# Performance work log

Measured on AMD Instinct MI355X. Metric: run time of the kernel, lower is better.

Reference implementation:

```python
import jax, jax.numpy as jnp
import numpy as np

B, T, C = 4, 128, 512
NH, HS = 8, 64          # n_head, head_dim = C // NH
ORDER = 3               # attention_order
SCALE = 1.0 / np.sqrt(HS)


def setup_inputs() -> dict:
    key = jax.random.key(0)
    ks = jax.random.split(key, 7)
    s = 0.02
    return {
        "x": jax.random.normal(ks[0], (B, T, C), jnp.float32),
        "Wp0": jax.random.normal(ks[1], (C, C), jnp.float32) * s,
        "Wp1": jax.random.normal(ks[2], (C, C), jnp.float32) * s,
        "Wp2": jax.random.normal(ks[3], (C, C), jnp.float32) * s,
        "Wv0": jax.random.normal(ks[4], (HS, HS), jnp.float32) * s,
        "Wv1": jax.random.normal(ks[5], (HS, HS), jnp.float32) * s,
        "Wc": jax.random.normal(ks[6], (C, C), jnp.float32) * s,
    }


def _heads(x, W):
    # Linear then split heads: (B,T,C) -> (B,NH,T,HS)
    return (x @ W).reshape(B, T, NH, HS).transpose(0, 2, 1, 3)


def _causal_mask(t, order):
    # indices grid [T]^order, True where i0 >= i1 >= ... >= i_{order-1}
    idx = jnp.arange(t)
    g = jnp.stack(jnp.meshgrid(*([idx] * order), indexing='ij'), axis=-1)
    return jnp.all(jnp.diff(g, axis=-1) <= 0, axis=-1)


def reference(x, Wp0, Wp1, Wp2, Wv0, Wv1, Wc):
    p0 = _heads(x, Wp0)  # (B,NH,T,HS)
    p1 = _heads(x, Wp1)
    p2 = _heads(x, Wp2)

    # pairwise scores, then higher-order broadcast exactly as the torch einsum
    # ('bh...i,bhkd->bh...ik' sums the key over d and broadcasts — faithful).
    att = jnp.einsum('bhid,bhjd->bhij', p0, p1) * SCALE        # (B,NH,T,T)
    att = jnp.einsum('bh...i,bhkd->bh...ik', att, p2)          # (B,NH,T,T,T)

    mask = _causal_mask(T, ORDER)[None, None]                  # (1,1,T,T,T)
    att = jnp.where(mask, att, -jnp.inf)
    att = jax.nn.softmax(att.reshape(B, NH, T, T * T), axis=-1)

    # value tensors with broadcasted elementwise product over the order dims
    V0 = (p1 @ Wv0)[:, :, :, None, :]   # (B,NH,T,1,HS)
    V1 = (p2 @ Wv1)[:, :, None, :, :]   # (B,NH,1,T,HS)
    V = (V0 * V1).reshape(B, NH, T * T, HS)

    y = jnp.einsum('bhij,bhjd->bhid', att, V)                  # (B,NH,T,HS)
    y = y.transpose(0, 2, 1, 3).reshape(B, T, C)
    return y @ Wc
```

## Files before the change

kernel.cpp:

```cpp
#include <hip/hip_runtime.h>
#include <hip/hip_bf16.h>
#include <math.h>

#define B 4
#define T 128
#define C 512
#define NH 8
#define HS 64
#define BH (B*NH)

typedef __attribute__((ext_vector_type(8))) short bf16x8;
typedef __attribute__((ext_vector_type(4))) float f32x4;

__device__ __forceinline__ unsigned short bfc(float x) {
    return __builtin_bit_cast(unsigned short, __float2bfloat16(x));
}
__device__ __forceinline__ float b2f(unsigned short u) {
    unsigned int x = ((unsigned int)u) << 16;
    return __builtin_bit_cast(float, x);
}
__device__ __forceinline__ unsigned int pk_bf16(float a, float b) {
    return (unsigned int)bfc(a) | ((unsigned int)bfc(b) << 16);
}
__device__ __forceinline__ float lo_f(unsigned int g) {
    return __builtin_bit_cast(float, g << 16);
}
__device__ __forceinline__ float hi_f(unsigned int g) {
    return __builtin_bit_cast(float, g & 0xffff0000u);
}

__global__ __launch_bounds__(256) void prep_kernel(
    const float* __restrict__ X, const float* __restrict__ Wp0, const float* __restrict__ Wp1,
    const float* __restrict__ Wp2, const float* __restrict__ Wc,
    const float* __restrict__ Wv0, const float* __restrict__ Wv1,
    unsigned short* __restrict__ Xb, unsigned short* __restrict__ W0T, unsigned short* __restrict__ W1T,
    unsigned short* __restrict__ W2T, unsigned short* __restrict__ WcT,
    unsigned short* __restrict__ We0T, unsigned short* __restrict__ We1T)
{
    __shared__ float Ls[64][69];
    __shared__ float As[16][68];
    __shared__ float Bs[16][68];
    const int z = blockIdx.z;
    const int tid = threadIdx.x;
    if (z == 0) {
        const int r0 = blockIdx.y * 64, c0 = blockIdx.x * 64;
        #pragma unroll
        for (int it = 0; it < 2; ++it) {
            const int q = tid + it * 256;
            const int row = q >> 3, c8 = (q & 7) * 8;
            const float4 a = *(const float4*)&X[(size_t)(r0 + row) * 512 + c0 + c8];
            const float4 b = *(const float4*)&X[(size_t)(r0 + row) * 512 + c0 + c8 + 4];
            uint4 o;
            o.x = pk_bf16(a.x, a.y);
            o.y = pk_bf16(a.z, a.w);
            o.z = pk_bf16(b.x, b.y);
            o.w = pk_bf16(b.z, b.w);
            *(uint4*)&Xb[(size_t)(r0 + row) * 512 + c0 + c8] = o;
        }
        return;
    }
    if (z <= 4) {
        const int r0 = blockIdx.y * 64, c0 = blockIdx.x * 64;
        const float* W = (z == 1) ? Wp0 : (z == 2) ? Wp1 : (z == 3) ? Wp2 : Wc;
        unsigned short* WT = (z == 1) ? W0T : (z == 2) ? W1T : (z == 3) ? W2T : WcT;
        #pragma unroll
        for (int it = 0; it < 4; ++it) {
            const int q = tid + it * 256;
            const int row = q >> 4, c4 = (q & 15) * 4;
            const float4 v = *(const float4*)&W[(size_t)(r0 + row) * 512 + c0 + c4];
            Ls[row][c4 + 0] = v.x; Ls[row][c4 + 1] = v.y; Ls[row][c4 + 2] = v.z; Ls[row][c4 + 3] = v.w;
        }
        __syncthreads();
        #pragma unroll
        for (int it = 0; it < 2; ++it) {
            const int q = tid + it * 256;
            const int nrow = q >> 3, k8 = (q & 7) * 8;
            uint4 o;
            o.x = pk_bf16(Ls[k8 + 0][nrow], Ls[k8 + 1][nrow]);
            o.y = pk_bf16(Ls[k8 + 2][nrow], Ls[k8 + 3][nrow]);
            o.z = pk_bf16(Ls[k8 + 4][nrow], Ls[k8 + 5][nrow]);
            o.w = pk_bf16(Ls[k8 + 6][nrow], Ls[k8 + 7][nrow]);
            *(uint4*)&WT[(size_t)(c0 + nrow) * 512 + r0 + k8] = o;
        }
        return;
    }
    const float* A  = (z == 5) ? Wp1 : Wp2;
    const float* Wv = (z == 5) ? Wv0 : Wv1;
    unsigned short* O = (z == 5) ? We0T : We1T;
    const int h = blockIdx.x;
    const int m0 = blockIdx.y * 64;
    const int tx = tid & 15, ty = tid >> 4;
    const int arow = tid >> 2, acol = (tid & 3) * 4;
    const int brow = tid >> 4, bcol = (tid & 15) * 4;
    float acc[4][4] = {};
    for (int k0 = 0; k0 < 64; k0 += 16) {
        const float4 av = *(const float4*)&A[(size_t)(m0 + arow) * 512 + h * 64 + k0 + acol];
        const float4 bv = *(const float4*)&Wv[(size_t)(k0 + brow) * 64 + bcol];
        __syncthreads();
        As[acol + 0][arow] = av.x; As[acol + 1][arow] = av.y;
        As[acol + 2][arow] = av.z; As[acol + 3][arow] = av.w;
        *(float4*)&Bs[brow][bcol] = bv;
        __syncthreads();
        #pragma unroll
        for (int kk = 0; kk < 16; ++kk) {
            const float4 a4 = *(const float4*)&As[kk][ty * 4];
            const float4 b4 = *(const float4*)&Bs[kk][tx * 4];
            const float ar[4] = {a4.x, a4.y, a4.z, a4.w};
            const float br[4] = {b4.x, b4.y, b4.z, b4.w};
            #pragma unroll
            for (int r = 0; r < 4; ++r)
                #pragma unroll
                for (int c = 0; c < 4; ++c)
                    acc[r][c] = fmaf(ar[r], br[c], acc[r][c]);
        }
    }
    #pragma unroll
    for (int r = 0; r < 4; ++r)
        #pragma unroll
        for (int c = 0; c < 4; ++c)
            O[(size_t)(h * 64 + tx * 4 + c) * 512 + (m0 + ty * 4 + r)] = bfc(acc[r][c]);
}

__global__ __launch_bounds__(256) void projmm_kernel(
    const unsigned short* __restrict__ Xb,
    const unsigned short* __restrict__ W0T, const unsigned short* __restrict__ W1T,
    const unsigned short* __restrict__ W2T,
    const unsigned short* __restrict__ We0T, const unsigned short* __restrict__ We1T,
    unsigned short* __restrict__ p0b, unsigned short* __restrict__ p1b,
    unsigned short* __restrict__ V0T, unsigned short* __restrict__ V1T, float* __restrict__ rr)
{
    __shared__ __align__(16) unsigned short As[64][72];
    __shared__ __align__(16) unsigned short Bs[64][72];
    __shared__ float sRS[4][64];
    const int z = blockIdx.z;
    const unsigned short* WT = (z == 0) ? W0T : (z == 1) ? W1T : (z == 2) ? W2T : (z == 3) ? We0T : We1T;
    const int m0 = blockIdx.y * 64, n0 = blockIdx.x * 64;
    const int tid = threadIdx.x;
    const int w = tid >> 6, lane = tid & 63, quad = lane >> 4, l16 = lane & 15;
    f32x4 acc[4];
    #pragma unroll
    for (int mt = 0; mt < 4; ++mt) acc[mt] = (f32x4){0.f, 0.f, 0.f, 0.f};
    for (int k0 = 0; k0 < 512; k0 += 64) {
        __syncthreads();
        #pragma unroll
        for (int it = 0; it < 2; ++it) {
            const int q = tid + it * 256;
            const int row = q >> 3, c8 = (q & 7) * 8;
            *(uint4*)&As[row][c8] = *(const uint4*)&Xb[(size_t)(m0 + row) * 512 + k0 + c8];
            *(uint4*)&Bs[row][c8] = *(const uint4*)&WT[(size_t)(n0 + row) * 512 + k0 + c8];
        }
        __syncthreads();
        #pragma unroll
        for (int kt = 0; kt < 2; ++kt) {
            const bf16x8 b8 = *(const bf16x8*)&Bs[w * 16 + l16][kt * 32 + quad * 8];
            #pragma unroll
            for (int mt = 0; mt < 4; ++mt) {
                const bf16x8 a8 = *(const bf16x8*)&As[mt * 16 + l16][kt * 32 + quad * 8];
                acc[mt] = __builtin_amdgcn_mfma_f32_16x16x32_bf16(a8, b8, acc[mt], 0, 0, 0);
            }
        }
    }
    if (z == 2) {
        #pragma unroll
        for (int mt = 0; mt < 4; ++mt)
            #pragma unroll
            for (int r = 0; r < 4; ++r) {
                float v = acc[mt][r];
                v += __shfl_xor(v, 1, 64); v += __shfl_xor(v, 2, 64);
                v += __shfl_xor(v, 4, 64); v += __shfl_xor(v, 8, 64);
                if (l16 == 0) sRS[w][mt * 16 + quad * 4 + r] = v;
            }
        __syncthreads();
        if (tid < 64) {
            const float s = sRS[0][tid] + sRS[1][tid] + sRS[2][tid] + sRS[3][tid];
            const int m = m0 + tid, b = m >> 7, tl = m & 127, h = n0 >> 6;
            rr[(b * NH + h) * T + tl] = s;
        }
        return;
    }
    const int n = n0 + w * 16 + l16;
    const int h = n >> 6, d = n & 63;
    #pragma unroll
    for (int mt = 0; mt < 4; ++mt) {
        #pragma unroll
        for (int r = 0; r < 4; ++r) {
            const int m = m0 + mt * 16 + quad * 4 + r;
            const int b = m >> 7, t = m & 127;
            const size_t hm = (size_t)(b * NH + h) * T + t;
            const float v = acc[mt][r];
            if (z == 0)      p0b[hm * HS + d] = bfc(v);
            else if (z == 1) p1b[hm * HS + d] = bfc(v);
            else if (z == 3) V0T[((size_t)(b * NH + h) * HS + d) * T + t] = bfc(v);
            else             V1T[((size_t)(b * NH + h) * HS + d) * T + t] = bfc(v);
        }
    }
}

__global__ __launch_bounds__(256) void attn_kernel(
    const unsigned short* __restrict__ p0b, const unsigned short* __restrict__ p1b,
    const float* __restrict__ rr, const unsigned short* __restrict__ V0Tg,
    const unsigned short* __restrict__ V1Tg, unsigned short* __restrict__ Yb)
{
    __shared__ __align__(16) unsigned short sE[128 * 64];
    __shared__ float sS[128];
    __shared__ float srr[128];
    __shared__ float sZ[4];

    const int blk = blockIdx.x;
    const int bh = blk & (BH - 1);
    const int i = (T - 1) - (blk >> 5);
    const int tid = threadIdx.x;
    const int w = tid >> 6;
    const int lane = tid & 63;
    const int quad = lane >> 4;
    const int l16 = lane & 15;

    if (tid < 128) srr[tid] = rr[bh * T + tid];

    uint4 v1r[4];
    {
        const unsigned short* src = V1Tg + ((size_t)bh * HS + (w << 4) + l16) * T + (quad << 3);
        #pragma unroll
        for (int kt = 0; kt < 4; ++kt) v1r[kt] = *(const uint4*)(src + (kt << 5));
    }

    {
        const unsigned short* ap = p0b + ((size_t)bh * T + i) * HS + (quad << 3);
        const unsigned short* bp = p1b + (size_t)bh * T * HS + (quad << 3);
        f32x4 s0 = (f32x4){0.f, 0.f, 0.f, 0.f};
        f32x4 s1 = (f32x4){0.f, 0.f, 0.f, 0.f};
        #pragma unroll
        for (int kt = 0; kt < 2; ++kt) {
            const bf16x8 a8 = *(const bf16x8*)(ap + (kt << 5));
            const bf16x8 b0 = *(const bf16x8*)(bp + (size_t)((w << 5) + l16) * HS + (kt << 5));
            const bf16x8 b1 = *(const bf16x8*)(bp + (size_t)((w << 5) + 16 + l16) * HS + (kt << 5));
            s0 = __builtin_amdgcn_mfma_f32_16x16x32_bf16(a8, b0, s0, 0, 0, 0);
            s1 = __builtin_amdgcn_mfma_f32_16x16x32_bf16(a8, b1, s1, 0, 0, 0);
        }
        if (quad == 0) {
            sS[(w << 5) + l16]      = s0[0] * 0.125f;
            sS[(w << 5) + 16 + l16] = s1[0] * 0.125f;
        }
    }
    __syncthreads();

    float mhat;
    {
        float s0 = (lane <= i) ? fabsf(sS[lane]) : 0.f;
        float s1 = (64 + lane <= i) ? fabsf(sS[64 + lane]) : 0.f;
        float r0 = (lane <= i) ? fabsf(srr[lane]) : 0.f;
        float r1 = (64 + lane <= i) ? fabsf(srr[64 + lane]) : 0.f;
        float aS = fmaxf(s0, s1), aR = fmaxf(r0, r1);
        #pragma unroll
        for (int off = 32; off; off >>= 1) {
            aS = fmaxf(aS, __shfl_xor(aS, off, 64));
            aR = fmaxf(aR, __shfl_xor(aR, off, 64));
        }
        mhat = aS * aR;
    }

    const float L2E = 1.4426950408889634f;
    const float bexp = -mhat * L2E;
    const int mtmax = i >> 4;
    const int cc = tid & 7;
    const int rowin = tid >> 3;
    const int k0l = cc << 3;
    float zacc = 0.f;

    float rk[8];
    *(float4*)&rk[0] = *(const float4*)&srr[k0l];
    *(float4*)&rk[4] = *(const float4*)&srr[k0l + 4];
    const int npass0 = (mtmax >> 1) + 1;
    for (int p = 0; p < npass0; ++p) {
        const int jj = (p << 5) + rowin;
        uint4 o = {0u, 0u, 0u, 0u};
        if (jj <= i && k0l <= jj) {
            const float aL = sS[jj] * L2E;
            const int dlim = jj - k0l;
            float e[8];
            #pragma unroll
            for (int q = 0; q < 8; ++q) {
                const float ex = __builtin_amdgcn_exp2f(fmaf(aL, rk[q], bexp));
                e[q] = (q <= dlim) ? ex : 0.f;
                zacc += e[q];
            }
            o.x = pk_bf16(e[0], e[1]);
            o.y = pk_bf16(e[2], e[3]);
            o.z = pk_bf16(e[4], e[5]);
            o.w = pk_bf16(e[6], e[7]);
        }
        *(uint4*)&sE[(jj << 6) + ((cc ^ (jj & 7)) << 3)] = o;
    }

    f32x4 acc[8];
    #pragma unroll
    for (int mt = 0; mt < 8; ++mt) acc[mt] = (f32x4){0.f, 0.f, 0.f, 0.f};

    if (mtmax < 4) {
        #pragma unroll
        for (int off = 32; off; off >>= 1) zacc += __shfl_xor(zacc, off, 64);
        if (lane == 0) sZ[w] = zacc;
        __syncthreads();
        #pragma unroll
        for (int mt = 0; mt < 4; ++mt) {
            if (mt <= mtmax) {
                #pragma unroll
                for (int kt = 0; kt <= 1; ++kt) {
                    if (kt <= (mt >> 1)) {
                        const int swz = ((kt << 2) + quad) ^ (l16 & 7);
                        const bf16x8 a8 = *(const bf16x8*)&sE[(((mt << 4) + l16) << 6) + (swz << 3)];
                        acc[mt] = __builtin_amdgcn_mfma_f32_16x16x32_bf16(
                            a8, __builtin_bit_cast(bf16x8, v1r[kt]), acc[mt], 0, 0, 0);
                    }
                }
            }
        }
    } else {
        __syncthreads();
        #pragma unroll
        for (int mt = 0; mt < 8; ++mt) {
            if (mt <= mtmax) {
                #pragma unroll
                for (int kt = 0; kt <= 1; ++kt) {
                    if (kt <= (mt >> 1)) {
                        const int swz = ((kt << 2) + quad) ^ (l16 & 7);
                        const bf16x8 a8 = *(const bf16x8*)&sE[(((mt << 4) + l16) << 6) + (swz << 3)];
                        acc[mt] = __builtin_amdgcn_mfma_f32_16x16x32_bf16(
                            a8, __builtin_bit_cast(bf16x8, v1r[kt]), acc[mt], 0, 0, 0);
                    }
                }
            }
        }
        __syncthreads();
        *(float4*)&rk[0] = *(const float4*)&srr[64 + k0l];
        *(float4*)&rk[4] = *(const float4*)&srr[64 + k0l + 4];
        const int npass1 = ((mtmax - 4) >> 1) + 1;
        for (int p = 0; p < npass1; ++p) {
            const int jj = 64 + (p << 5) + rowin;
            uint4 o = {0u, 0u, 0u, 0u};
            if (jj <= i && 64 + k0l <= jj) {
                const float aL = sS[jj] * L2E;
                const int dlim = jj - 64 - k0l;
                float e[8];
                #pragma unroll
                for (int q = 0; q < 8; ++q) {
                    const float ex = __builtin_amdgcn_exp2f(fmaf(aL, rk[q], bexp));
                    e[q] = (q <= dlim) ? ex : 0.f;
                    zacc += e[q];
                }
                o.x = pk_bf16(e[0], e[1]);
                o.y = pk_bf16(e[2], e[3]);
                o.z = pk_bf16(e[4], e[5]);
                o.w = pk_bf16(e[6], e[7]);
            }
            *(uint4*)&sE[(jj << 6) + ((cc ^ (jj & 7)) << 3)] = o;
        }
        #pragma unroll
        for (int off = 32; off; off >>= 1) zacc += __shfl_xor(zacc, off, 64);
        if (lane == 0) sZ[w] = zacc;
        __syncthreads();
        #pragma unroll
        for (int mt = 4; mt < 8; ++mt) {
            if (mt <= mtmax) {
                #pragma unroll
                for (int kt = 2; kt <= 3; ++kt) {
                    if (kt <= (mt >> 1)) {
                        const int swz = (((kt & 1) << 2) + quad) ^ (l16 & 7);
                        const bf16x8 a8 = *(const bf16x8*)&sE[(((mt << 4) + l16) << 6) + (swz << 3)];
                        acc[mt] = __builtin_amdgcn_mfma_f32_16x16x32_bf16(
                            a8, __builtin_bit_cast(bf16x8, v1r[kt]), acc[mt], 0, 0, 0);
                    }
                }
            }
        }
    }
    const float Z = sZ[0] + sZ[1] + sZ[2] + sZ[3];

    const unsigned short* v0t = V0Tg + ((size_t)bh * HS + (w << 4) + l16) * T;
    float part = 0.f;
    #pragma unroll
    for (int mt = 0; mt < 8; ++mt) {
        if (mt < mtmax) {
            const uint2 u = *(const uint2*)&v0t[(mt << 4) + (quad << 2)];
            part = fmaf(lo_f(u.x), acc[mt][0], part);
            part = fmaf(hi_f(u.x), acc[mt][1], part);
            part = fmaf(lo_f(u.y), acc[mt][2], part);
            part = fmaf(hi_f(u.y), acc[mt][3], part);
        } else if (mt == mtmax) {
            const uint2 u = *(const uint2*)&v0t[(mt << 4) + (quad << 2)];
            const int jb = (mt << 4) + (quad << 2);
            if (jb + 0 <= i) part = fmaf(lo_f(u.x), acc[mt][0], part);
            if (jb + 1 <= i) part = fmaf(hi_f(u.x), acc[mt][1], part);
            if (jb + 2 <= i) part = fmaf(lo_f(u.y), acc[mt][2], part);
            if (jb + 3 <= i) part = fmaf(hi_f(u.y), acc[mt][3], part);
        }
    }
    part += __shfl_xor(part, 16, 64);
    part += __shfl_xor(part, 32, 64);
    if (lane < 16) {
        const int bb = bh >> 3, hh = bh & 7;
        Yb[((size_t)(bb * T + i) * C) + hh * HS + (w << 4) + l16] = bfc(part / Z);
    }
}

__global__ __launch_bounds__(256) void outmm_kernel(
    const unsigned short* __restrict__ Ab, const unsigned short* __restrict__ WT,
    float* __restrict__ OUT)
{
    __shared__ __align__(16) unsigned short As[64][72];
    __shared__ __align__(16) unsigned short Bs[64][72];
    const int m0 = blockIdx.y * 64, n0 = blockIdx.x * 64;
    const int tid = threadIdx.x;
    const int w = tid >> 6, lane = tid & 63, quad = lane >> 4, l16 = lane & 15;
    f32x4 acc[4];
    #pragma unroll
    for (int mt = 0; mt < 4; ++mt) acc[mt] = (f32x4){0.f, 0.f, 0.f, 0.f};
    for (int k0 = 0; k0 < 512; k0 += 64) {
        __syncthreads();
        #pragma unroll
        for (int it = 0; it < 2; ++it) {
            const int q = tid + it * 256;
            const int row = q >> 3, c8 = (q & 7) * 8;
            *(uint4*)&As[row][c8] = *(const uint4*)&Ab[(size_t)(m0 + row) * 512 + k0 + c8];
            *(uint4*)&Bs[row][c8] = *(const uint4*)&WT[(size_t)(n0 + row) * 512 + k0 + c8];
        }
        __syncthreads();
        #pragma unroll
        for (int kt = 0; kt < 2; ++kt) {
            const bf16x8 b8 = *(const bf16x8*)&Bs[w * 16 + l16][kt * 32 + quad * 8];
            #pragma unroll
            for (int mt = 0; mt < 4; ++mt) {
                const bf16x8 a8 = *(const bf16x8*)&As[mt * 16 + l16][kt * 32 + quad * 8];
                acc[mt] = __builtin_amdgcn_mfma_f32_16x16x32_bf16(a8, b8, acc[mt], 0, 0, 0);
            }
        }
    }
    const int n = n0 + w * 16 + l16;
    #pragma unroll
    for (int mt = 0; mt < 4; ++mt)
        #pragma unroll
        for (int r = 0; r < 4; ++r) {
            const int mrow = m0 + mt * 16 + quad * 4 + r;
            OUT[(size_t)mrow * 512 + n] = acc[mt][r];
        }
}

extern "C" void kernel_launch(void* const* d_in, const int* in_sizes, int n_in,
                              void* d_out, int out_size, void* d_ws, size_t ws_size,
                              hipStream_t stream)
{
    const float* x   = (const float*)d_in[0];
    const float* Wp0 = (const float*)d_in[1];
    const float* Wp1 = (const float*)d_in[2];
    const float* Wp2 = (const float*)d_in[3];
    const float* Wv0 = (const float*)d_in[4];
    const float* Wv1 = (const float*)d_in[5];
    const float* Wc  = (const float*)d_in[6];
    float* out = (float*)d_out;

    char* w8 = (char*)d_ws;
    const size_t HB = 512 * 1024;
    unsigned short* Xb   = (unsigned short*)(w8 + 0 * HB);
    unsigned short* W0T  = (unsigned short*)(w8 + 1 * HB);
    unsigned short* W1T  = (unsigned short*)(w8 + 2 * HB);
    unsigned short* W2T  = (unsigned short*)(w8 + 3 * HB);
    unsigned short* WcT  = (unsigned short*)(w8 + 4 * HB);
    unsigned short* We0T = (unsigned short*)(w8 + 5 * HB);
    unsigned short* We1T = (unsigned short*)(w8 + 6 * HB);
    unsigned short* p0b  = (unsigned short*)(w8 + 7 * HB);
    unsigned short* p1b  = (unsigned short*)(w8 + 8 * HB);
    unsigned short* V0T  = (unsigned short*)(w8 + 9 * HB);
    unsigned short* V1T  = (unsigned short*)(w8 + 10 * HB);
    unsigned short* Yb   = (unsigned short*)(w8 + 11 * HB);
    float*          rr   = (float*)        (w8 + 12 * HB);

    prep_kernel  <<<dim3(8, 8, 7), 256, 0, stream>>>(x, Wp0, Wp1, Wp2, Wc, Wv0, Wv1,
                                                     Xb, W0T, W1T, W2T, WcT, We0T, We1T);
    projmm_kernel<<<dim3(8, 8, 5), 256, 0, stream>>>(Xb, W0T, W1T, W2T, We0T, We1T,
                                                     p0b, p1b, V0T, V1T, rr);
    attn_kernel  <<<dim3(BH * T), 256, 0, stream>>>(p0b, p1b, rr, V0T, V1T, Yb);
    outmm_kernel <<<dim3(8, 8), 256, 0, stream>>>(Yb, WcT, out);
}
```

Baseline: 123.2 us.

## Process eight query rows per attention block with balanced row pairing

The attention kernel now handles eight query rows per block instead of one, shrinking the grid from 4096 to 512 blocks. The score MFMA computes all eight rows' scores at once, filling otherwise wasted MFMA rows, and the V1 register load is amortized across rows. Rows are picked in mirrored pairs (ig and 15-ig within alternating 16-row groups) so per-block causal work is balanced. The trade-off is less parallelism, with only 512 blocks on a many-CU GPU, and each block runs a serial loop over its rows with extra block-wide barriers.

```diff
diff --git a/kernel.cpp b/kernel.cpp
--- a/kernel.cpp
+++ b/kernel.cpp
@@ -202,13 +202,13 @@
     const unsigned short* __restrict__ V1Tg, unsigned short* __restrict__ Yb)
 {
     __shared__ __align__(16) unsigned short sE[128 * 64];
-    __shared__ float sS[128];
+    __shared__ float sS[8][128];
     __shared__ float srr[128];
     __shared__ float sZ[4];
 
-    const int blk = blockIdx.x;
-    const int bh = blk & (BH - 1);
-    const int i = (T - 1) - (blk >> 5);
+    const int bid = blockIdx.x;
+    const int bh = bid & (BH - 1);
+    const int ig = bid >> 5;
     const int tid = threadIdx.x;
     const int w = tid >> 6;
     const int lane = tid & 63;
@@ -225,7 +225,9 @@
     }
 
     {
-        const unsigned short* ap = p0b + ((size_t)bh * T + i) * HS + (quad << 3);
+        const int qr = l16 & 7;
+        const int irow = (qr & 1) ? (16 * qr + 15 - ig) : (16 * qr + ig);
+        const unsigned short* ap = p0b + ((size_t)bh * T + irow) * HS + (quad << 3);
         const unsigned short* bp = p1b + (size_t)bh * T * HS + (quad << 3);
         f32x4 s0 = (f32x4){0.f, 0.f, 0.f, 0.f};
         f32x4 s1 = (f32x4){0.f, 0.f, 0.f, 0.f};
@@ -237,110 +239,55 @@
             s0 = __builtin_amdgcn_mfma_f32_16x16x32_bf16(a8, b0, s0, 0, 0, 0);
             s1 = __builtin_amdgcn_mfma_f32_16x16x32_bf16(a8, b1, s1, 0, 0, 0);
         }
-        if (quad == 0) {
-            sS[(w << 5) + l16]      = s0[0] * 0.125f;
-            sS[(w << 5) + 16 + l16] = s1[0] * 0.125f;
+        if (quad < 2) {
+            #pragma unroll
+            for (int r = 0; r < 4; ++r) {
+                sS[quad * 4 + r][(w << 5) + l16]      = s0[r] * 0.125f;
+                sS[quad * 4 + r][(w << 5) + 16 + l16] = s1[r] * 0.125f;
+            }
         }
     }
     __syncthreads();
 
-    float mhat;
-    {
-        float s0 = (lane <= i) ? fabsf(sS[lane]) : 0.f;
-        float s1 = (64 + lane <= i) ? fabsf(sS[64 + lane]) : 0.f;
-        float r0 = (lane <= i) ? fabsf(srr[lane]) : 0.f;
-        float r1 = (64 + lane <= i) ? fabsf(srr[64 + lane]) : 0.f;
-        float aS = fmaxf(s0, s1), aR = fmaxf(r0, r1);
-        #pragma unroll
-        for (int off = 32; off; off >>= 1) {
-            aS = fmaxf(aS, __shfl_xor(aS, off, 64));
-            aR = fmaxf(aR, __shfl_xor(aR, off, 64));
-        }
-        mhat = aS * aR;
-    }
-
+    const unsigned short* v0t = V0Tg + ((size_t)bh * HS + (w << 4) + l16) * T;
     const float L2E = 1.4426950408889634f;
-    const float bexp = -mhat * L2E;
-    const int mtmax = i >> 4;
-    const int cc = tid & 7;
-    const int rowin = tid >> 3;
-    const int k0l = cc << 3;
-    float zacc = 0.f;
-
-    float rk[8];
-    *(float4*)&rk[0] = *(const float4*)&srr[k0l];
-    *(float4*)&rk[4] = *(const float4*)&srr[k0l + 4];
-    const int npass0 = (mtmax >> 1) + 1;
-    for (int p = 0; p < npass0; ++p) {
-        const int jj = (p << 5) + rowin;
-        uint4 o = {0u, 0u, 0u, 0u};
-        if (jj <= i && k0l <= jj) {
-            const float aL = sS[jj] * L2E;
-            const int dlim = jj - k0l;
-            float e[8];
-            #pragma unroll
-            for (int q = 0; q < 8; ++q) {
-                const float ex = __builtin_amdgcn_exp2f(fmaf(aL, rk[q], bexp));
-                e[q] = (q <= dlim) ? ex : 0.f;
-                zacc += e[q];
-            }
-            o.x = pk_bf16(e[0], e[1]);
-            o.y = pk_bf16(e[2], e[3]);
-            o.z = pk_bf16(e[4], e[5]);
-            o.w = pk_bf16(e[6], e[7]);
-        }
-        *(uint4*)&sE[(jj << 6) + ((cc ^ (jj & 7)) << 3)] = o;
-    }
-
-    f32x4 acc[8];
-    #pragma unroll
-    for (int mt = 0; mt < 8; ++mt) acc[mt] = (f32x4){0.f, 0.f, 0.f, 0.f};
-
-    if (mtmax < 4) {
-        #pragma unroll
-        for (int off = 32; off; off >>= 1) zacc += __shfl_xor(zacc, off, 64);
-        if (lane == 0) sZ[w] = zacc;
-        __syncthreads();
-        #pragma unroll
-        for (int mt = 0; mt < 4; ++mt) {
-            if (mt <= mtmax) {
-                #pragma unroll
-                for (int kt = 0; kt <= 1; ++kt) {
-                    if (kt <= (mt >> 1)) {
-                        const int swz = ((kt << 2) + quad) ^ (l16 & 7);
-                        const bf16x8 a8 = *(const bf16x8*)&sE[(((mt << 4) + l16) << 6) + (swz << 3)];
-                        acc[mt] = __builtin_amdgcn_mfma_f32_16x16x32_bf16(
-                            a8, __builtin_bit_cast(bf16x8, v1r[kt]), acc[mt], 0, 0, 0);
-                    }
-                }
-            }
-        }
-    } else {
-        __syncthreads();
-        #pragma unroll
-        for (int mt = 0; mt < 8; ++mt) {
-            if (mt <= mtmax) {
-                #pragma unroll
-                for (int kt = 0; kt <= 1; ++kt) {
-                    if (kt <= (mt >> 1)) {
-                        const int swz = ((kt << 2) + quad) ^ (l16 & 7);
-                        const bf16x8 a8 = *(const bf16x8*)&sE[(((mt << 4) + l16) << 6) + (swz << 3)];
-                        acc[mt] = __builtin_amdgcn_mfma_f32_16x16x32_bf16(
-                            a8, __builtin_bit_cast(bf16x8, v1r[kt]), acc[mt], 0, 0, 0);
-                    }
-                }
-            }
-        }
-        __syncthreads();
-        *(float4*)&rk[0] = *(const float4*)&srr[64 + k0l];
-        *(float4*)&rk[4] = *(const float4*)&srr[64 + k0l + 4];
-        const int npass1 = ((mtmax - 4) >> 1) + 1;
-        for (int p = 0; p < npass1; ++p) {
-            const int jj = 64 + (p << 5) + rowin;
+
+    for (int qq = 7; qq >= 0; --qq) {
+        const int i = (qq & 1) ? (16 * qq + 15 - ig) : (16 * qq + ig);
+        const float* sSq = sS[qq];
+
+        float mhat;
+        {
+            float a0 = (lane <= i) ? fabsf(sSq[lane]) : 0.f;
+            float a1 = (64 + lane <= i) ? fabsf(sSq[64 + lane]) : 0.f;
+            float r0 = (lane <= i) ? fabsf(srr[lane]) : 0.f;
+            float r1 = (64 + lane <= i) ? fabsf(srr[64 + lane]) : 0.f;
+            float aS = fmaxf(a0, a1), aR = fmaxf(r0, r1);
+            #pragma unroll
+            for (int off = 32; off; off >>= 1) {
+                aS = fmaxf(aS, __shfl_xor(aS, off, 64));
+                aR = fmaxf(aR, __shfl_xor(aR, off, 64));
+            }
+            mhat = aS * aR;
+        }
+
+        const float bexp = -mhat * L2E;
+        const int mtmax = i >> 4;
+        const int cc = tid & 7;
+        const int rowin = tid >> 3;
+        const int k0l = cc << 3;
+        float zacc = 0.f;
+
+        float rk[8];
+        *(float4*)&rk[0] = *(const float4*)&srr[k0l];
+        *(float4*)&rk[4] = *(const float4*)&srr[k0l + 4];
+        const int npass0 = (mtmax >> 1) + 1;
+        for (int p = 0; p < npass0; ++p) {
+            const int jj = (p << 5) + rowin;
             uint4 o = {0u, 0u, 0u, 0u};
-            if (jj <= i && 64 + k0l <= jj) {
-                const float aL = sS[jj] * L2E;
-                const int dlim = jj - 64 - k0l;
+            if (jj <= i && k0l <= jj) {
+                const float aL = sSq[jj] * L2E;
+                const int dlim = jj - k0l;
                 float e[8];
                 #pragma unroll
                 for (int q = 0; q < 8; ++q) {
@@ -355,51 +302,116 @@
             }
             *(uint4*)&sE[(jj << 6) + ((cc ^ (jj & 7)) << 3)] = o;
         }
-        #pragma unroll
-        for (int off = 32; off; off >>= 1) zacc += __shfl_xor(zacc, off, 64);
-        if (lane == 0) sZ[w] = zacc;
-        __syncthreads();
-        #pragma unroll
-        for (int mt = 4; mt < 8; ++mt) {
-            if (mt <= mtmax) {
-                #pragma unroll
-                for (int kt = 2; kt <= 3; ++kt) {
-                    if (kt <= (mt >> 1)) {
-                        const int swz = (((kt & 1) << 2) + quad) ^ (l16 & 7);
-                        const bf16x8 a8 = *(const bf16x8*)&sE[(((mt << 4) + l16) << 6) + (swz << 3)];
-                        acc[mt] = __builtin_amdgcn_mfma_f32_16x16x32_bf16(
-                            a8, __builtin_bit_cast(bf16x8, v1r[kt]), acc[mt], 0, 0, 0);
+
+        f32x4 acc[8];
+        #pragma unroll
+        for (int mt = 0; mt < 8; ++mt) acc[mt] = (f32x4){0.f, 0.f, 0.f, 0.f};
+
+        if (mtmax < 4) {
+            #pragma unroll
+            for (int off = 32; off; off >>= 1) zacc += __shfl_xor(zacc, off, 64);
+            if (lane == 0) sZ[w] = zacc;
+            __syncthreads();
+            #pragma unroll
+            for (int mt = 0; mt < 4; ++mt) {
+                if (mt <= mtmax) {
+                    #pragma unroll
+                    for (int kt = 0; kt <= 1; ++kt) {
+                        if (kt <= (mt >> 1)) {
+                            const int swz = ((kt << 2) + quad) ^ (l16 & 7);
+                            const bf16x8 a8 = *(const bf16x8*)&sE[(((mt << 4) + l16) << 6) + (swz << 3)];
+                            acc[mt] = __builtin_amdgcn_mfma_f32_16x16x32_bf16(
+                                a8, __builtin_bit_cast(bf16x8, v1r[kt]), acc[mt], 0, 0, 0);
+                        }
                     }
                 }
             }
-        }
-    }
-    const float Z = sZ[0] + sZ[1] + sZ[2] + sZ[3];
-
-    const unsigned short* v0t = V0Tg + ((size_t)bh * HS + (w << 4) + l16) * T;
-    float part = 0.f;
-    #pragma unroll
-    for (int mt = 0; mt < 8; ++mt) {
-        if (mt < mtmax) {
-            const uint2 u = *(const uint2*)&v0t[(mt << 4) + (quad << 2)];
-            part = fmaf(lo_f(u.x), acc[mt][0], part);
-            part = fmaf(hi_f(u.x), acc[mt][1], part);
-            part = fmaf(lo_f(u.y), acc[mt][2], part);
-            part = fmaf(hi_f(u.y), acc[mt][3], part);
-        } else if (mt == mtmax) {
-            const uint2 u = *(const uint2*)&v0t[(mt << 4) + (quad << 2)];
-            const int jb = (mt << 4) + (quad << 2);
-            if (jb + 0 <= i) part = fmaf(lo_f(u.x), acc[mt][0], part);
-            if (jb + 1 <= i) part = fmaf(hi_f(u.x), acc[mt][1], part);
-            if (jb + 2 <= i) part = fmaf(lo_f(u.y), acc[mt][2], part);
-            if (jb + 3 <= i) part = fmaf(hi_f(u.y), acc[mt][3], part);
-        }
-    }
-    part += __shfl_xor(part, 16, 64);
-    part += __shfl_xor(part, 32, 64);
-    if (lane < 16) {
-        const int bb = bh >> 3, hh = bh & 7;
-        Yb[((size_t)(bb * T + i) * C) + hh * HS + (w << 4) + l16] = bfc(part / Z);
+        } else {
+            __syncthreads();
+            #pragma unroll
+            for (int mt = 0; mt < 8; ++mt) {
+                if (mt <= mtmax) {
+                    #pragma unroll
+                    for (int kt = 0; kt <= 1; ++kt) {
+                        if (kt <= (mt >> 1)) {
+                            const int swz = ((kt << 2) + quad) ^ (l16 & 7);
+                            const bf16x8 a8 = *(const bf16x8*)&sE[(((mt << 4) + l16) << 6) + (swz << 3)];
+                            acc[mt] = __builtin_amdgcn_mfma_f32_16x16x32_bf16(
+                                a8, __builtin_bit_cast(bf16x8, v1r[kt]), acc[mt], 0, 0, 0);
+                        }
+                    }
+                }
+            }
+            __syncthreads();
+            *(float4*)&rk[0] = *(const float4*)&srr[64 + k0l];
+            *(float4*)&rk[4] = *(const float4*)&srr[64 + k0l + 4];
+            const int npass1 = ((mtmax - 4) >> 1) + 1;
+            for (int p = 0; p < npass1; ++p) {
+                const int jj = 64 + (p << 5) + rowin;
+                uint4 o = {0u, 0u, 0u, 0u};
+                if (jj <= i && 64 + k0l <= jj) {
+                    const float aL = sSq[jj] * L2E;
+                    const int dlim = jj - 64 - k0l;
+                    float e[8];
+                    #pragma unroll
+                    for (int q = 0; q < 8; ++q) {
+                        const float ex = __builtin_amdgcn_exp2f(fmaf(aL, rk[q], bexp));
+                        e[q] = (q <= dlim) ? ex : 0.f;
+                        zacc += e[q];
+                    }
+                    o.x = pk_bf16(e[0], e[1]);
+                    o.y = pk_bf16(e[2], e[3]);
+                    o.z = pk_bf16(e[4], e[5]);
+                    o.w = pk_bf16(e[6], e[7]);
+                }
+                *(uint4*)&sE[(jj << 6) + ((cc ^ (jj & 7)) << 3)] = o;
+            }
+            #pragma unroll
+            for (int off = 32; off; off >>= 1) zacc += __shfl_xor(zacc, off, 64);
+            if (lane == 0) sZ[w] = zacc;
+            __syncthreads();
+            #pragma unroll
+            for (int mt = 4; mt < 8; ++mt) {
+                if (mt <= mtmax) {
+                    #pragma unroll
+                    for (int kt = 2; kt <= 3; ++kt) {
+                        if (kt <= (mt >> 1)) {
+                            const int swz = (((kt & 1) << 2) + quad) ^ (l16 & 7);
+                            const bf16x8 a8 = *(const bf16x8*)&sE[(((mt << 4) + l16) << 6) + (swz << 3)];
+                            acc[mt] = __builtin_amdgcn_mfma_f32_16x16x32_bf16(
+                                a8, __builtin_bit_cast(bf16x8, v1r[kt]), acc[mt], 0, 0, 0);
+                        }
+                    }
+                }
+            }
+        }
+        const float Z = sZ[0] + sZ[1] + sZ[2] + sZ[3];
+
+        float part = 0.f;
+        #pragma unroll
+        for (int mt = 0; mt < 8; ++mt) {
+            if (mt < mtmax) {
+                const uint2 u = *(const uint2*)&v0t[(mt << 4) + (quad << 2)];
+                part = fmaf(lo_f(u.x), acc[mt][0], part);
+                part = fmaf(hi_f(u.x), acc[mt][1], part);
+                part = fmaf(lo_f(u.y), acc[mt][2], part);
+                part = fmaf(hi_f(u.y), acc[mt][3], part);
+            } else if (mt == mtmax) {
+                const uint2 u = *(const uint2*)&v0t[(mt << 4) + (quad << 2)];
+                const int jb = (mt << 4) + (quad << 2);
+                if (jb + 0 <= i) part = fmaf(lo_f(u.x), acc[mt][0], part);
+                if (jb + 1 <= i) part = fmaf(hi_f(u.x), acc[mt][1], part);
+                if (jb + 2 <= i) part = fmaf(lo_f(u.y), acc[mt][2], part);
+                if (jb + 3 <= i) part = fmaf(hi_f(u.y), acc[mt][3], part);
+            }
+        }
+        part += __shfl_xor(part, 16, 64);
+        part += __shfl_xor(part, 32, 64);
+        if (lane < 16) {
+            const int bb = bh >> 3, hh = bh & 7;
+            Yb[((size_t)(bb * T + i) * C) + hh * HS + (w << 4) + l16] = bfc(part / Z);
+        }
+        __syncthreads();
     }
 }
 
@@ -478,6 +490,6 @@
                                                      Xb, W0T, W1T, W2T, WcT, We0T, We1T);
     projmm_kernel<<<dim3(8, 8, 5), 256, 0, stream>>>(Xb, W0T, W1T, W2T, We0T, We1T,
                                                      p0b, p1b, V0T, V1T, rr);
-    attn_kernel  <<<dim3(BH * T), 256, 0, stream>>>(p0b, p1b, rr, V0T, V1T, Yb);
+    attn_kernel  <<<dim3(512), 256, 0, stream>>>(p0b, p1b, rr, V0T, V1T, Yb);
     outmm_kernel <<<dim3(8, 8), 256, 0, stream>>>(Yb, WcT, out);
 }
```

Measured after the change: 120.9 us. Within noise of the previous version (-1.9%).
